# Performance work log

Hardware: AMD Instinct MI355X
Metric: run time of the kernel (lower is better)

The kernel has to match this reference:

```python
import jax, jax.numpy as jnp
import numpy as np

NUM_EXPERTS = 8
TOP_K = 2


def setup_inputs() -> dict:
    key = jax.random.key(0)
    ks = jax.random.split(key, 5)
    B, T, D, H, E = 8, 4096, 512, 1536, NUM_EXPERTS
    scale = 0.02
    x = jax.random.normal(ks[0], (B, T, D), dtype=jnp.float32)
    gate_w = jax.random.normal(ks[1], (E, D), dtype=jnp.float32) * scale
    w1 = jax.random.normal(ks[2], (E, H, D), dtype=jnp.float32) * scale
    w3 = jax.random.normal(ks[3], (E, H, D), dtype=jnp.float32) * scale
    w2 = jax.random.normal(ks[4], (E, D, H), dtype=jnp.float32) * scale
    return {"x": x, "gate_w": gate_w, "w1": w1, "w3": w3, "w2": w2}


def reference(x, gate_w, w1, w3, w2):
    B, T, D = x.shape
    E = gate_w.shape[0]
    xf = x.reshape(-1, D)                      # [N, D], N = B*T
    N = xf.shape[0]
    gate_logits = xf @ gate_w.T                # [N, E]
    weights, indices = jax.lax.top_k(gate_logits, TOP_K)   # [N, K]
    weights = jax.nn.softmax(weights, axis=-1)
    # combine[n, e] = sum_k weights[n, k] * (indices[n, k] == e)
    combine = jnp.zeros((N, E), dtype=xf.dtype).at[
        jnp.arange(N)[:, None], indices].add(weights)       # [N, E]
    out = jnp.zeros_like(xf)
    for e in range(E):  # small fixed expert count
        h = jax.nn.silu(xf @ w1[e].T) * (xf @ w3[e].T)      # [N, H]
        y = h @ w2[e].T                                     # [N, D]
        out = out + combine[:, e:e + 1] * y
    return out.reshape(B, T, D)
```

## Files before the change

### kernel.cpp

```cpp
#include <hip/hip_runtime.h>


#define N_TOK 32768
#define DIM   512
#define HID   1536
#define NE    8
#define MTS   256

typedef __attribute__((ext_vector_type(8))) short  short8;
typedef __attribute__((ext_vector_type(4))) float  floatx4;

#define MFMA(a,b,c) __builtin_amdgcn_mfma_f32_16x16x32_bf16(a,b,c,0,0,0)

__device__ __forceinline__ unsigned short f2bf(float f) {
  unsigned int u = __float_as_uint(f);
  u += 0x7fffu + ((u >> 16) & 1u);
  return (unsigned short)(u >> 16);
}
__device__ __forceinline__ unsigned pk2(float a, float b) {
  return (unsigned)f2bf(a) | ((unsigned)f2bf(b) << 16);
}
__device__ __forceinline__ void gl_lds16(const unsigned short* g, unsigned short* l) {
  __builtin_amdgcn_global_load_lds(
      (const __attribute__((address_space(1))) unsigned int*)g,
      (__attribute__((address_space(3))) unsigned int*)l, 16, 0, 0);
}

__global__ void __launch_bounds__(256) cvt3_kernel(const float* __restrict__ w1,
                                                   const float* __restrict__ w3,
                                                   const float* __restrict__ w2,
                                                   unsigned short* __restrict__ w1b,
                                                   unsigned short* __restrict__ w3b,
                                                   unsigned short* __restrict__ w2b,
                                                   int n4) {
  int i = blockIdx.x * 256 + threadIdx.x;
  const float* s; unsigned short* d; int j = i;
  if (j < n4)          { s = w1; d = w1b; }
  else if (j < 2 * n4) { s = w3; d = w3b; j -= n4; }
  else                 { s = w2; d = w2b; j -= 2 * n4; }
  float4 v = ((const float4*)s)[j];
  uint2 o; o.x = pk2(v.x, v.y); o.y = pk2(v.z, v.w);
  ((uint2*)d)[j] = o;
}

__global__ void __launch_bounds__(256) gate1_kernel(const float* __restrict__ x,
                                                    const float* __restrict__ gw,
                                                    unsigned short* __restrict__ xb,
                                                    unsigned* __restrict__ eidx,
                                                    float* __restrict__ wts) {
  int lane = threadIdx.x & 63;
  int wave = threadIdx.x >> 6;
  int t = blockIdx.x * 4 + wave;

  const float4* xp = (const float4*)(x + (size_t)t * DIM + lane * 8);
  float4 x0 = xp[0], x1 = xp[1];

  uint4 o; o.x = pk2(x0.x, x0.y); o.y = pk2(x0.z, x0.w);
  o.z = pk2(x1.x, x1.y); o.w = pk2(x1.z, x1.w);
  *(uint4*)(xb + (size_t)t * DIM + lane * 8) = o;

  double p[NE];
#pragma unroll
  for (int e = 0; e < NE; ++e) {
    const float4* gp = (const float4*)(gw + e * DIM + lane * 8);
    float4 g0 = gp[0], g1 = gp[1];
    p[e] = (double)x0.x * g0.x + (double)x0.y * g0.y + (double)x0.z * g0.z + (double)x0.w * g0.w
         + (double)x1.x * g1.x + (double)x1.y * g1.y + (double)x1.z * g1.z + (double)x1.w * g1.w;
  }
#pragma unroll
  for (int m = 1; m < 64; m <<= 1) {
#pragma unroll
    for (int e = 0; e < NE; ++e) p[e] += __shfl_xor(p[e], m);
  }
  if (lane == 0) {
    double m1 = -1e300, m2 = -1e300; int i1 = 0, i2 = 0;
#pragma unroll
    for (int e = 0; e < NE; ++e) {
      double v = p[e];
      if (v > m1) { m2 = m1; i2 = i1; m1 = v; i1 = e; }
      else if (v > m2) { m2 = v; i2 = e; }
    }
    float e2 = __expf((float)(m2 - m1));
    float wa = 1.f / (1.f + e2);
    eidx[t] = (unsigned)i1 | ((unsigned)i2 << 8);
    wts[t]  = wa;
  }
}

__global__ void __launch_bounds__(256) gate2a_kernel(const unsigned* __restrict__ eidx,
                                                     int* __restrict__ cnt) {
  __shared__ unsigned histP[NE], histS[NE];
  int tid = threadIdx.x;
  if (tid < NE) { histP[tid] = 0; histS[tid] = 0; }
  __syncthreads();
  int t0 = blockIdx.x * 1024;
#pragma unroll
  for (int i = 0; i < 4; ++i) {
    unsigned pk = eidx[t0 + tid + i * 256];
    atomicAdd(&histP[pk & 0xff], 1u);
    atomicAdd(&histS[(pk >> 8) & 0xff], 1u);
  }
  __syncthreads();
  if (tid < NE) {
    atomicAdd(&cnt[tid], (int)histP[tid]);
    atomicAdd(&cnt[NE + tid], (int)histS[tid]);
  }
}

__global__ void __launch_bounds__(256) gate2b_kernel(const unsigned* __restrict__ eidx,
                                                     const float* __restrict__ wts,
                                                     int* __restrict__ tokl,
                                                     float* __restrict__ wgtl,
                                                     int* __restrict__ cnt) {
  __shared__ unsigned histP[NE], histS[NE];
  __shared__ unsigned baseP[NE], baseS[NE];
  int tid = threadIdx.x;
  if (tid < NE) { histP[tid] = 0; histS[tid] = 0; }
  __syncthreads();
  int t0 = blockIdx.x * 1024;
  unsigned pk[4]; float wv[4];
#pragma unroll
  for (int i = 0; i < 4; ++i) {
    int t = t0 + tid + i * 256;
    pk[i] = eidx[t]; wv[i] = wts[t];
    atomicAdd(&histP[pk[i] & 0xff], 1u);
    atomicAdd(&histS[(pk[i] >> 8) & 0xff], 1u);
  }
  __syncthreads();
  if (tid < NE) {
    baseP[tid] = (unsigned)atomicAdd(&cnt[2 * NE + tid], (int)histP[tid]);
    baseS[tid] = (unsigned)cnt[tid] + (unsigned)atomicAdd(&cnt[3 * NE + tid], (int)histS[tid]);
    histP[tid] = 0; histS[tid] = 0;
  }
  __syncthreads();
#pragma unroll
  for (int i = 0; i < 4; ++i) {
    int t = t0 + tid + i * 256;
    int e1 = pk[i] & 0xff, e2 = (pk[i] >> 8) & 0xff;
    unsigned p1 = baseP[e1] + atomicAdd(&histP[e1], 1u);
    tokl[e1 * N_TOK + p1] = t; wgtl[e1 * N_TOK + p1] = wv[i];
    unsigned p2 = baseS[e2] + atomicAdd(&histS[e2], 1u);
    tokl[e2 * N_TOK + p2] = t | (int)0x80000000; wgtl[e2 * N_TOK + p2] = 1.f - wv[i];
  }
}

__global__ void __launch_bounds__(256, 4) ffn1_kernel(
    const unsigned short* __restrict__ xb,
    const unsigned short* __restrict__ w1b,
    const unsigned short* __restrict__ w3b,
    const int* __restrict__ tokl, const float* __restrict__ wgtl,
    const int* __restrict__ cnt,
    unsigned short* __restrict__ Hs,
    int h0base, int P, int NT) {
  int e  = blockIdx.x & 7;
  int t  = blockIdx.x >> 3;
  int nt = t % NT, mt = t / NT;
  int ne = cnt[e] + cnt[NE + e];
  int m0 = mt * 128;
  if (m0 >= ne) return;
  int offs = 0;
#pragma unroll
  for (int i = 0; i < NE; ++i) offs += (i < e) ? (cnt[i] + cnt[NE + i]) : 0;

  __shared__ __align__(16) unsigned short As[128 * 64];
  __shared__ __align__(16) unsigned short Bs[128 * 64];

  int tid = threadIdx.x, w = tid >> 6, lane = tid & 63;
  int quad = lane >> 4, l16 = lane & 15;
  int wm = w >> 1, wn = w & 1;

  int rl = lane >> 3, cc = (lane & 7) ^ rl;
  const unsigned short* pa[4];
#pragma unroll
  for (int i = 0; i < 4; ++i) {
    int r = m0 + 32 * w + 8 * i + rl;
    int tok = tokl[e * N_TOK + (r < ne ? r : m0)] & 0x7fffffff;
    pa[i] = xb + (size_t)tok * DIM + cc * 8;
  }
  const unsigned short* wsrc = (w < 2) ? w1b : w3b;
  const unsigned short* pb0 =
      wsrc + ((size_t)e * HID + h0base + nt * 64 + ((32 * w) & 63) + rl) * DIM + cc * 8;

  floatx4 u[4][2], v[4][2];
#pragma unroll
  for (int i = 0; i < 4; ++i)
#pragma unroll
    for (int j = 0; j < 2; ++j) { u[i][j] = (floatx4){0,0,0,0}; v[i][j] = (floatx4){0,0,0,0}; }

  for (int k0 = 0; k0 < DIM; k0 += 64) {
#pragma unroll
    for (int i = 0; i < 4; ++i) {
      gl_lds16(pa[i], &As[(32 * w + 8 * i) * 64]);
      gl_lds16(pb0 + (size_t)i * 8 * DIM, &Bs[(32 * w + 8 * i) * 64]);
      pa[i] += 64;
    }
    pb0 += 64;
    __syncthreads();
#pragma unroll
    for (int kk = 0; kk < 2; ++kk) {
      int s = ((4 * kk + quad) ^ (l16 & 7)) * 8;
      short8 a[4], b1[2], b3[2];
#pragma unroll
      for (int i = 0; i < 4; ++i)
        a[i] = *(const short8*)&As[(wm * 64 + i * 16 + l16) * 64 + s];
#pragma unroll
      for (int j = 0; j < 2; ++j) {
        b1[j] = *(const short8*)&Bs[(wn * 32 + j * 16 + l16) * 64 + s];
        b3[j] = *(const short8*)&Bs[(64 + wn * 32 + j * 16 + l16) * 64 + s];
      }
#pragma unroll
      for (int i = 0; i < 4; ++i)
#pragma unroll
        for (int j = 0; j < 2; ++j) {
          u[i][j] = MFMA(a[i], b1[j], u[i][j]);
          v[i][j] = MFMA(a[i], b3[j], v[i][j]);
        }
    }
    __syncthreads();
  }

#pragma unroll
  for (int i = 0; i < 4; ++i)
#pragma unroll
    for (int r = 0; r < 4; ++r) {
      int tr = wm * 64 + i * 16 + quad * 4 + r;
      float wg = wgtl[e * N_TOK + m0 + tr];
#pragma unroll
      for (int j = 0; j < 2; ++j) {
        int hc = wn * 32 + j * 16 + l16;
        float uu = u[i][j][r], vv = v[i][j][r];
        float h = (uu / (1.f + __expf(-uu))) * vv * wg;
        As[tr * 64 + hc] = f2bf(h);
      }
    }
  __syncthreads();
  {
    int row = tid >> 1, half = tid & 1;
    if (m0 + row < ne) {
      const unsigned short* s = &As[row * 64 + half * 32];
      unsigned short* d = Hs + (size_t)(offs + m0 + row) * P + nt * 64 + half * 32;
#pragma unroll
      for (int j = 0; j < 4; ++j) *(uint4*)(d + j * 8) = *(const uint4*)(s + j * 8);
    }
  }
}

__global__ void __launch_bounds__(256, 4) ffn2_kernel(
    const unsigned short* __restrict__ Hs,
    const unsigned short* __restrict__ w2b,
    const int* __restrict__ tokl, const int* __restrict__ cnt,
    float* __restrict__ out,
    int h0base, int P, int first, int cls) {
  int e  = blockIdx.x & 7;
  int t  = blockIdx.x >> 3;
  int nt = t & 3, mt = t >> 2;
  int neP = cnt[e];
  int neAll = neP + cnt[NE + e];
  int m0 = mt * 128;
  if (cls == 0) { if (m0 >= neP) return; }
  else          { if (m0 >= neAll || m0 + 128 <= neP) return; }
  int offs = 0;
#pragma unroll
  for (int i = 0; i < NE; ++i) offs += (i < e) ? (cnt[i] + cnt[NE + i]) : 0;

  __shared__ __align__(16) unsigned short As[128 * 64];
  __shared__ __align__(16) unsigned short Bs[128 * 64];

  int tid = threadIdx.x, w = tid >> 6, lane = tid & 63;
  int quad = lane >> 4, l16 = lane & 15;
  int wm = w >> 1, wn = w & 1;

  int rl = lane >> 3, cc = (lane & 7) ^ rl;
  int dbase = nt * 128;
  const unsigned short* pa0 = Hs + (size_t)(offs + m0 + 32 * w + rl) * P + cc * 8;
  const unsigned short* pb0 =
      w2b + ((size_t)e * DIM + dbase + 32 * w + rl) * HID + h0base + cc * 8;

  floatx4 acc[4][4];
#pragma unroll
  for (int i = 0; i < 4; ++i)
#pragma unroll
    for (int j = 0; j < 4; ++j) acc[i][j] = (floatx4){0, 0, 0, 0};

  for (int k0 = 0; k0 < P; k0 += 64) {
#pragma unroll
    for (int i = 0; i < 4; ++i) {
      gl_lds16(pa0 + (size_t)i * 8 * P,   &As[(32 * w + 8 * i) * 64]);
      gl_lds16(pb0 + (size_t)i * 8 * HID, &Bs[(32 * w + 8 * i) * 64]);
    }
    pa0 += 64; pb0 += 64;
    __syncthreads();
#pragma unroll
    for (int kk = 0; kk < 2; ++kk) {
      int s = ((4 * kk + quad) ^ (l16 & 7)) * 8;
      short8 a[4], b[4];
#pragma unroll
      for (int i = 0; i < 4; ++i) {
        a[i] = *(const short8*)&As[(wm * 64 + i * 16 + l16) * 64 + s];
        b[i] = *(const short8*)&Bs[(wn * 64 + i * 16 + l16) * 64 + s];
      }
#pragma unroll
      for (int i = 0; i < 4; ++i)
#pragma unroll
        for (int j = 0; j < 4; ++j)
          acc[i][j] = MFMA(a[i], b[j], acc[i][j]);
    }
    __syncthreads();
  }

#pragma unroll
  for (int i = 0; i < 4; ++i)
#pragma unroll
    for (int r = 0; r < 4; ++r) {
      int row = wm * 64 + i * 16 + quad * 4 + r;
      int gr = m0 + row;
      int tk = tokl[e * N_TOK + gr];
      bool doit = cls ? (gr < neAll && tk < 0) : (gr < neP);
      if (!doit) continue;
      float* dst = out + (size_t)(tk & 0x7fffffff) * DIM + dbase + wn * 64 + l16;
      if (first && cls == 0) {
#pragma unroll
        for (int j = 0; j < 4; ++j) dst[j * 16] = acc[i][j][r];
      } else {
#pragma unroll
        for (int j = 0; j < 4; ++j) dst[j * 16] += acc[i][j][r];
      }
    }
}

extern "C" void kernel_launch(void* const* d_in, const int* in_sizes, int n_in,
                              void* d_out, int out_size, void* d_ws, size_t ws_size,
                              hipStream_t stream) {
  const float* x  = (const float*)d_in[0];
  const float* gw = (const float*)d_in[1];
  const float* w1 = (const float*)d_in[2];
  const float* w3 = (const float*)d_in[3];
  const float* w2 = (const float*)d_in[4];
  float* out = (float*)d_out;

  const size_t NW = (size_t)NE * HID * DIM;
  char* p = (char*)d_ws;
  unsigned short* w1b = (unsigned short*)p;  p += NW * 2;
  unsigned short* w3b = (unsigned short*)p;  p += NW * 2;
  unsigned short* w2b = (unsigned short*)p;  p += NW * 2;
  unsigned short* xb  = (unsigned short*)p;  p += (size_t)N_TOK * DIM * 2;
  int*      tokl = (int*)p;       p += (size_t)NE * N_TOK * 4;
  float*    wgtl = (float*)p;     p += (size_t)NE * N_TOK * 4;
  unsigned* eidx = (unsigned*)p;  p += (size_t)N_TOK * 4;
  float*    wts  = (float*)p;     p += (size_t)N_TOK * 4;
  int*      cnt  = (int*)p;       p += 256;
  unsigned short* Hs = (unsigned short*)p;
  size_t fixed = (size_t)(p - (char*)d_ws);
  if (ws_size < fixed) return;
  size_t avail = ws_size - fixed;

  const int cands[5] = {1536, 768, 512, 384, 256};
  int P = 0;
  for (int i = 0; i < 5; ++i)
    if ((size_t)(2 * N_TOK + 128) * cands[i] * 2 <= avail) { P = cands[i]; break; }
  if (!P) return;

  hipMemsetAsync(cnt, 0, 256, stream);

  int n4 = (int)(NW / 4);
  cvt3_kernel<<<3 * n4 / 256, 256, 0, stream>>>(w1, w3, w2, w1b, w3b, w2b, n4);

  gate1_kernel<<<N_TOK / 4, 256, 0, stream>>>(x, gw, xb, eidx, wts);
  gate2a_kernel<<<N_TOK / 1024, 256, 0, stream>>>(eidx, cnt);
  gate2b_kernel<<<N_TOK / 1024, 256, 0, stream>>>(eidx, wts, tokl, wgtl, cnt);

  int pass = 0;
  for (int h0 = 0; h0 < HID; h0 += P) {
    int NT = P / 64;
    ffn1_kernel<<<8 * MTS * NT, 256, 0, stream>>>(xb, w1b, w3b, tokl, wgtl, cnt, Hs, h0, P, NT);
    ffn2_kernel<<<8 * MTS * 4, 256, 0, stream>>>(Hs, w2b, tokl, cnt, out, h0, P, pass == 0, 0);
    ffn2_kernel<<<8 * MTS * 4, 256, 0, stream>>>(Hs, w2b, tokl, cnt, out, h0, P, 0, 1);
    ++pass;
  }
}
```

Before: 663.5 us.

## Enlarge FFN GEMM tiles: 128-wide hidden tiles in ffn1, 256-row tiles in ffn2

```diff
diff --git a/kernel.cpp b/kernel.cpp
--- a/kernel.cpp
+++ b/kernel.cpp
@@ -6,6 +6,7 @@
 #define HID   1536
 #define NE    8
 #define MTS   256
+#define MT2   128
 
 typedef __attribute__((ext_vector_type(8))) short  short8;
 typedef __attribute__((ext_vector_type(4))) float  floatx4;
@@ -144,7 +145,7 @@
   }
 }
 
-__global__ void __launch_bounds__(256, 4) ffn1_kernel(
+__global__ void __launch_bounds__(256, 2) ffn1_kernel(
     const unsigned short* __restrict__ xb,
     const unsigned short* __restrict__ w1b,
     const unsigned short* __restrict__ w3b,
@@ -162,8 +163,9 @@
 #pragma unroll
   for (int i = 0; i < NE; ++i) offs += (i < e) ? (cnt[i] + cnt[NE + i]) : 0;
 
-  __shared__ __align__(16) unsigned short As[128 * 64];
-  __shared__ __align__(16) unsigned short Bs[128 * 64];
+  __shared__ __align__(16) unsigned short lds[24576];
+  unsigned short* As = lds;
+  unsigned short* Bs = lds + 128 * 64;
 
   int tid = threadIdx.x, w = tid >> 6, lane = tid & 63;
   int quad = lane >> 4, l16 = lane & 15;
@@ -177,41 +179,43 @@
     int tok = tokl[e * N_TOK + (r < ne ? r : m0)] & 0x7fffffff;
     pa[i] = xb + (size_t)tok * DIM + cc * 8;
   }
-  const unsigned short* wsrc = (w < 2) ? w1b : w3b;
-  const unsigned short* pb0 =
-      wsrc + ((size_t)e * HID + h0base + nt * 64 + ((32 * w) & 63) + rl) * DIM + cc * 8;
-
-  floatx4 u[4][2], v[4][2];
+  const unsigned short* pb1 =
+      w1b + ((size_t)e * HID + h0base + nt * 128 + 32 * w + rl) * DIM + cc * 8;
+  const unsigned short* pb3 =
+      w3b + ((size_t)e * HID + h0base + nt * 128 + 32 * w + rl) * DIM + cc * 8;
+
+  floatx4 u[4][4], v[4][4];
 #pragma unroll
   for (int i = 0; i < 4; ++i)
 #pragma unroll
-    for (int j = 0; j < 2; ++j) { u[i][j] = (floatx4){0,0,0,0}; v[i][j] = (floatx4){0,0,0,0}; }
+    for (int j = 0; j < 4; ++j) { u[i][j] = (floatx4){0,0,0,0}; v[i][j] = (floatx4){0,0,0,0}; }
 
   for (int k0 = 0; k0 < DIM; k0 += 64) {
 #pragma unroll
     for (int i = 0; i < 4; ++i) {
       gl_lds16(pa[i], &As[(32 * w + 8 * i) * 64]);
-      gl_lds16(pb0 + (size_t)i * 8 * DIM, &Bs[(32 * w + 8 * i) * 64]);
+      gl_lds16(pb1 + (size_t)i * 8 * DIM, &Bs[(32 * w + 8 * i) * 64]);
+      gl_lds16(pb3 + (size_t)i * 8 * DIM, &Bs[(128 + 32 * w + 8 * i) * 64]);
       pa[i] += 64;
     }
-    pb0 += 64;
+    pb1 += 64; pb3 += 64;
     __syncthreads();
 #pragma unroll
     for (int kk = 0; kk < 2; ++kk) {
       int s = ((4 * kk + quad) ^ (l16 & 7)) * 8;
-      short8 a[4], b1[2], b3[2];
+      short8 a[4], b1[4], b3[4];
 #pragma unroll
       for (int i = 0; i < 4; ++i)
         a[i] = *(const short8*)&As[(wm * 64 + i * 16 + l16) * 64 + s];
 #pragma unroll
-      for (int j = 0; j < 2; ++j) {
-        b1[j] = *(const short8*)&Bs[(wn * 32 + j * 16 + l16) * 64 + s];
-        b3[j] = *(const short8*)&Bs[(64 + wn * 32 + j * 16 + l16) * 64 + s];
+      for (int j = 0; j < 4; ++j) {
+        b1[j] = *(const short8*)&Bs[(wn * 64 + j * 16 + l16) * 64 + s];
+        b3[j] = *(const short8*)&Bs[(128 + wn * 64 + j * 16 + l16) * 64 + s];
       }
 #pragma unroll
       for (int i = 0; i < 4; ++i)
 #pragma unroll
-        for (int j = 0; j < 2; ++j) {
+        for (int j = 0; j < 4; ++j) {
           u[i][j] = MFMA(a[i], b1[j], u[i][j]);
           v[i][j] = MFMA(a[i], b3[j], v[i][j]);
         }
@@ -219,6 +223,7 @@
     __syncthreads();
   }
 
+  unsigned short* AsF = lds;
 #pragma unroll
   for (int i = 0; i < 4; ++i)
 #pragma unroll
@@ -226,26 +231,26 @@
       int tr = wm * 64 + i * 16 + quad * 4 + r;
       float wg = wgtl[e * N_TOK + m0 + tr];
 #pragma unroll
-      for (int j = 0; j < 2; ++j) {
-        int hc = wn * 32 + j * 16 + l16;
+      for (int j = 0; j < 4; ++j) {
+        int hc = wn * 64 + j * 16 + l16;
         float uu = u[i][j][r], vv = v[i][j][r];
         float h = (uu / (1.f + __expf(-uu))) * vv * wg;
-        As[tr * 64 + hc] = f2bf(h);
+        AsF[tr * 128 + hc] = f2bf(h);
       }
     }
   __syncthreads();
   {
     int row = tid >> 1, half = tid & 1;
     if (m0 + row < ne) {
-      const unsigned short* s = &As[row * 64 + half * 32];
-      unsigned short* d = Hs + (size_t)(offs + m0 + row) * P + nt * 64 + half * 32;
-#pragma unroll
-      for (int j = 0; j < 4; ++j) *(uint4*)(d + j * 8) = *(const uint4*)(s + j * 8);
-    }
-  }
-}
-
-__global__ void __launch_bounds__(256, 4) ffn2_kernel(
+      const unsigned short* s = &AsF[row * 128 + half * 64];
+      unsigned short* d = Hs + (size_t)(offs + m0 + row) * P + nt * 128 + half * 64;
+#pragma unroll
+      for (int j = 0; j < 8; ++j) *(uint4*)(d + j * 8) = *(const uint4*)(s + j * 8);
+    }
+  }
+}
+
+__global__ void __launch_bounds__(256, 2) ffn2_kernel(
     const unsigned short* __restrict__ Hs,
     const unsigned short* __restrict__ w2b,
     const int* __restrict__ tokl, const int* __restrict__ cnt,
@@ -256,15 +261,16 @@
   int nt = t & 3, mt = t >> 2;
   int neP = cnt[e];
   int neAll = neP + cnt[NE + e];
-  int m0 = mt * 128;
+  int m0 = mt * 256;
   if (cls == 0) { if (m0 >= neP) return; }
-  else          { if (m0 >= neAll || m0 + 128 <= neP) return; }
+  else          { if (m0 >= neAll || m0 + 256 <= neP) return; }
   int offs = 0;
 #pragma unroll
   for (int i = 0; i < NE; ++i) offs += (i < e) ? (cnt[i] + cnt[NE + i]) : 0;
 
-  __shared__ __align__(16) unsigned short As[128 * 64];
-  __shared__ __align__(16) unsigned short Bs[128 * 64];
+  __shared__ __align__(16) unsigned short lds[24576];
+  unsigned short* As = lds;
+  unsigned short* Bs = lds + 256 * 64;
 
   int tid = threadIdx.x, w = tid >> 6, lane = tid & 63;
   int quad = lane >> 4, l16 = lane & 15;
@@ -272,35 +278,37 @@
 
   int rl = lane >> 3, cc = (lane & 7) ^ rl;
   int dbase = nt * 128;
-  const unsigned short* pa0 = Hs + (size_t)(offs + m0 + 32 * w + rl) * P + cc * 8;
+  const unsigned short* pa0 = Hs + (size_t)(offs + m0 + 64 * w + rl) * P + cc * 8;
   const unsigned short* pb0 =
       w2b + ((size_t)e * DIM + dbase + 32 * w + rl) * HID + h0base + cc * 8;
 
-  floatx4 acc[4][4];
-#pragma unroll
-  for (int i = 0; i < 4; ++i)
+  floatx4 acc[8][4];
+#pragma unroll
+  for (int i = 0; i < 8; ++i)
 #pragma unroll
     for (int j = 0; j < 4; ++j) acc[i][j] = (floatx4){0, 0, 0, 0};
 
   for (int k0 = 0; k0 < P; k0 += 64) {
 #pragma unroll
-    for (int i = 0; i < 4; ++i) {
-      gl_lds16(pa0 + (size_t)i * 8 * P,   &As[(32 * w + 8 * i) * 64]);
+    for (int i = 0; i < 8; ++i)
+      gl_lds16(pa0 + (size_t)i * 8 * P, &As[(64 * w + 8 * i) * 64]);
+#pragma unroll
+    for (int i = 0; i < 4; ++i)
       gl_lds16(pb0 + (size_t)i * 8 * HID, &Bs[(32 * w + 8 * i) * 64]);
-    }
     pa0 += 64; pb0 += 64;
     __syncthreads();
 #pragma unroll
     for (int kk = 0; kk < 2; ++kk) {
       int s = ((4 * kk + quad) ^ (l16 & 7)) * 8;
-      short8 a[4], b[4];
-#pragma unroll
-      for (int i = 0; i < 4; ++i) {
-        a[i] = *(const short8*)&As[(wm * 64 + i * 16 + l16) * 64 + s];
-        b[i] = *(const short8*)&Bs[(wn * 64 + i * 16 + l16) * 64 + s];
-      }
-#pragma unroll
-      for (int i = 0; i < 4; ++i)
+      short8 a[8], b[4];
+#pragma unroll
+      for (int i = 0; i < 8; ++i)
+        a[i] = *(const short8*)&As[(wm * 128 + i * 16 + l16) * 64 + s];
+#pragma unroll
+      for (int j = 0; j < 4; ++j)
+        b[j] = *(const short8*)&Bs[(wn * 64 + j * 16 + l16) * 64 + s];
+#pragma unroll
+      for (int i = 0; i < 8; ++i)
 #pragma unroll
         for (int j = 0; j < 4; ++j)
           acc[i][j] = MFMA(a[i], b[j], acc[i][j]);
@@ -309,12 +317,12 @@
   }
 
 #pragma unroll
-  for (int i = 0; i < 4; ++i)
+  for (int i = 0; i < 8; ++i)
 #pragma unroll
     for (int r = 0; r < 4; ++r) {
-      int row = wm * 64 + i * 16 + quad * 4 + r;
+      int row = wm * 128 + i * 16 + quad * 4 + r;
       int gr = m0 + row;
-      int tk = tokl[e * N_TOK + gr];
+      int tk = tokl[e * N_TOK + (gr < neAll ? gr : 0)];
       bool doit = cls ? (gr < neAll && tk < 0) : (gr < neP);
       if (!doit) continue;
       float* dst = out + (size_t)(tk & 0x7fffffff) * DIM + dbase + wn * 64 + l16;
@@ -357,7 +365,7 @@
   const int cands[5] = {1536, 768, 512, 384, 256};
   int P = 0;
   for (int i = 0; i < 5; ++i)
-    if ((size_t)(2 * N_TOK + 128) * cands[i] * 2 <= avail) { P = cands[i]; break; }
+    if ((size_t)(2 * N_TOK + 512) * cands[i] * 2 <= avail) { P = cands[i]; break; }
   if (!P) return;
 
   hipMemsetAsync(cnt, 0, 256, stream);
@@ -371,10 +379,10 @@
 
   int pass = 0;
   for (int h0 = 0; h0 < HID; h0 += P) {
-    int NT = P / 64;
+    int NT = P / 128;
     ffn1_kernel<<<8 * MTS * NT, 256, 0, stream>>>(xb, w1b, w3b, tokl, wgtl, cnt, Hs, h0, P, NT);
-    ffn2_kernel<<<8 * MTS * 4, 256, 0, stream>>>(Hs, w2b, tokl, cnt, out, h0, P, pass == 0, 0);
-    ffn2_kernel<<<8 * MTS * 4, 256, 0, stream>>>(Hs, w2b, tokl, cnt, out, h0, P, 0, 1);
+    ffn2_kernel<<<8 * MT2 * 4, 256, 0, stream>>>(Hs, w2b, tokl, cnt, out, h0, P, pass == 0, 0);
+    ffn2_kernel<<<8 * MT2 * 4, 256, 0, stream>>>(Hs, w2b, tokl, cnt, out, h0, P, 0, 1);
     ++pass;
   }
 }
```

New measurement: 759.7 us. +14.5%, slower.
